# Performance work log

Measured on AMD Instinct MI355X. Metric: run time of the kernel, lower is better.

Reference implementation:

```python
import jax, jax.numpy as jnp
import numpy as np

T = 4096      # sentence length
V = 50257     # vocab size
E = 1024      # embedding dim
H = 512       # hidden per direction (hidden_dim // 2)
NT = 32       # tagset size


def setup_inputs() -> dict:
    key = jax.random.key(0)
    ks = jax.random.split(key, 12)
    s = 0.02
    return {
        "sentence": jax.random.randint(ks[0], (T,), 0, V, dtype=jnp.int32),
        "emb": jax.random.normal(ks[1], (V, E), jnp.float32) * s,
        "W_ih_f": jax.random.normal(ks[2], (3 * H, E), jnp.float32) * s,
        "W_hh_f": jax.random.normal(ks[3], (3 * H, H), jnp.float32) * s,
        "b_ih_f": jax.random.normal(ks[4], (3 * H,), jnp.float32) * s,
        "b_hh_f": jax.random.normal(ks[5], (3 * H,), jnp.float32) * s,
        "W_ih_b": jax.random.normal(ks[6], (3 * H, E), jnp.float32) * s,
        "W_hh_b": jax.random.normal(ks[7], (3 * H, H), jnp.float32) * s,
        "b_ih_b": jax.random.normal(ks[8], (3 * H,), jnp.float32) * s,
        "b_hh_b": jax.random.normal(ks[9], (3 * H,), jnp.float32) * s,
        "W_out": jax.random.normal(ks[10], (NT, E), jnp.float32) * s,
    }


def _gru_dir(x, W_ih, W_hh, b_ih, b_hh):
    """Run a single-direction GRU over x [T, E] -> hidden states [T, H].
    PyTorch GRU gate math: r,z,n order; h' = (1-z)*n + z*h; h0 = 0."""
    gi = x @ W_ih.T + b_ih  # [T, 3H] input projections, one big GEMM

    def step(h, gi_t):
        gh = h @ W_hh.T + b_hh            # [3H]
        ir, iz, inn = jnp.split(gi_t, 3)
        hr, hz, hn = jnp.split(gh, 3)
        r = jax.nn.sigmoid(ir + hr)
        z = jax.nn.sigmoid(iz + hz)
        n = jnp.tanh(inn + r * hn)
        h_new = (1.0 - z) * n + z * h
        return h_new, h_new

    h0 = jnp.zeros((W_hh.shape[1],), x.dtype)
    _, hs = jax.lax.scan(step, h0, gi)
    return hs  # [T, H]


def reference(sentence, emb, W_ih_f, W_hh_f, b_ih_f, b_hh_f,
              W_ih_b, W_hh_b, b_ih_b, b_hh_b, W_out):
    x = emb[sentence]  # [T, E] embedding lookup
    h_fwd = _gru_dir(x, W_ih_f, W_hh_f, b_ih_f, b_hh_f)            # [T, H]
    h_bwd = _gru_dir(x[::-1], W_ih_b, W_hh_b, b_ih_b, b_hh_b)[::-1]  # [T, H]
    h = jnp.concatenate([h_fwd, h_bwd], axis=-1)  # [T, 2H]
    return h @ W_out.T  # [T, NT] tag scores (no bias)
```

## Files before the change

kernel.cpp:

```cpp
#include <hip/hip_runtime.h>

#define T_LEN 4096
#define E_DIM 1024
#define H_DIM 512
#define NT_DIM 32
#define NG 3072
#define G_DIR 64
#define OPW 8

typedef __attribute__((ext_vector_type(8))) short bf16x8;
typedef __attribute__((ext_vector_type(4))) float f32x4;
typedef unsigned long long ull;

__device__ inline unsigned short f2bf(float f) {
    unsigned int u = __float_as_uint(f);
    unsigned int r = (u + 0x7fffu + ((u >> 16) & 1u)) >> 16;
    return (unsigned short)r;
}
__device__ inline float bf2f(unsigned short u) {
    return __uint_as_float(((unsigned int)u) << 16);
}
__device__ inline ull packhs(float v, unsigned tag) {
    return (ull)__float_as_uint(v) | ((ull)tag << 32);
}

__global__ void embed_cast(const int* __restrict__ sent, const float* __restrict__ emb,
                           unsigned short* __restrict__ xb) {
    int t = blockIdx.x;
    int row = sent[t];
    const float4* src = (const float4*)(emb + (size_t)row * E_DIM);
    ushort4* dst = (ushort4*)(xb + (size_t)t * E_DIM);
    float4 v = src[threadIdx.x];
    ushort4 o;
    o.x = f2bf(v.x); o.y = f2bf(v.y); o.z = f2bf(v.z); o.w = f2bf(v.w);
    dst[threadIdx.x] = o;
}

__global__ void wcast(const float* __restrict__ wf, const float* __restrict__ wb_,
                      unsigned short* __restrict__ w) {
    int r = blockIdx.x;
    const float* src = (r < 1536) ? (wf + (size_t)r * E_DIM) : (wb_ + (size_t)(r - 1536) * E_DIM);
    const float4* s4 = (const float4*)src;
    ushort4* dst = (ushort4*)(w + (size_t)r * E_DIM);
    float4 v = s4[threadIdx.x];
    ushort4 o;
    o.x = f2bf(v.x); o.y = f2bf(v.y); o.z = f2bf(v.z); o.w = f2bf(v.w);
    dst[threadIdx.x] = o;
}

#define LDST 40
__global__ __launch_bounds__(256) void gi_gemm(const unsigned short* __restrict__ xb,
                                               const unsigned short* __restrict__ wb,
                                               const float* __restrict__ bihf,
                                               const float* __restrict__ bihb,
                                               unsigned short* __restrict__ gi) {
    __shared__ __align__(16) unsigned short As[64 * LDST];
    __shared__ __align__(16) unsigned short Bs[64 * LDST];
    int tile_m = (blockIdx.x % 64) * 64;
    int tile_n = (blockIdx.x / 64) * 64;
    int tid = threadIdx.x;
    int lane = tid & 63, wv = tid >> 6;
    int quad = lane >> 4, r15 = lane & 15;
    int srow = tid >> 2, sseg = tid & 3;

    f32x4 acc[4] = {};
    for (int kb = 0; kb < E_DIM; kb += 32) {
        uint4 a = *(const uint4*)(xb + (size_t)(tile_m + srow) * E_DIM + kb + sseg * 8);
        uint4 b = *(const uint4*)(wb + (size_t)(tile_n + srow) * E_DIM + kb + sseg * 8);
        *(uint4*)&As[srow * LDST + sseg * 8] = a;
        *(uint4*)&Bs[srow * LDST + sseg * 8] = b;
        __syncthreads();
        bf16x8 af = *(bf16x8*)&As[(wv * 16 + r15) * LDST + quad * 8];
#pragma unroll
        for (int nt = 0; nt < 4; nt++) {
            bf16x8 bf = *(bf16x8*)&Bs[(nt * 16 + r15) * LDST + quad * 8];
            acc[nt] = __builtin_amdgcn_mfma_f32_16x16x32_bf16(af, bf, acc[nt], 0, 0, 0);
        }
        __syncthreads();
    }
#pragma unroll
    for (int nt = 0; nt < 4; nt++) {
        int gn = tile_n + nt * 16 + r15;
        float bias = (gn < 1536) ? bihf[gn] : bihb[gn - 1536];
#pragma unroll
        for (int rg = 0; rg < 4; rg++) {
            int gm = tile_m + wv * 16 + quad * 4 + rg;
            gi[(size_t)gm * NG + gn] = f2bf(acc[nt][rg] + bias);
        }
    }
}

__global__ __launch_bounds__(512) void gru_rec(
    const float* __restrict__ whhf, const float* __restrict__ bhhf,
    const float* __restrict__ whhb, const float* __restrict__ bhhb,
    const unsigned short* __restrict__ gi, ull* __restrict__ hxf, ull* __restrict__ hxb) {
    int wgid = blockIdx.x;
    int dir = wgid >> 6;
    int g = wgid & 63;
    const float* whh = dir ? whhb : whhf;
    const float* bhh = dir ? bhhb : bhhf;
    ull* hx = dir ? hxb : hxf;

    int tid = threadIdx.x;
    int kp = tid & 7;
    int q = tid >> 3;
    int kg = g * OPW + kp;
    int wave = tid >> 6;
    int lane = tid & 63;

    float4 wr[2], wz[2], wn[2];
    {
        const float4* pr_ = (const float4*)(whh + (size_t)kg * H_DIM + q * 8);
        const float4* pz_ = (const float4*)(whh + (size_t)(kg + 512) * H_DIM + q * 8);
        const float4* pn_ = (const float4*)(whh + (size_t)(kg + 1024) * H_DIM + q * 8);
        wr[0] = pr_[0]; wr[1] = pr_[1];
        wz[0] = pz_[0]; wz[1] = pz_[1];
        wn[0] = pn_[0]; wn[1] = pn_[1];
    }
    float bias_r = 0.f, bias_z = 0.f, bias_n = 0.f, h_own = 0.f;
    int kg0 = g * OPW + lane;
    if (wave == 0 && lane < OPW) {
        bias_r = bhh[kg0]; bias_z = bhh[kg0 + 512]; bias_n = bhh[kg0 + 1024];
    }

    __shared__ float hsh[512];
    __shared__ float part[3][8][OPW];
    hsh[tid] = 0.f;
    __syncthreads();

    float gir = 0.f, giz = 0.f, gin = 0.f;

    for (int s = 0; s < T_LEN; s++) {
        int row = dir ? (T_LEN - 1 - s) : s;
        if (wave == 0) {
            if (lane < OPW) {
                const unsigned short* gp = gi + (size_t)row * NG + dir * 1536 + kg0;
                gir = bf2f(gp[0]); giz = bf2f(gp[512]); gin = bf2f(gp[1024]);
            }
            if (s > 0) {
                int prow = dir ? (T_LEN - s) : (s - 1);
                const ull* rowp = hx + (size_t)prow * H_DIM;
                ull v[8];
                bool ok;
                do {
#pragma unroll
                    for (int i = 0; i < 8; i++)
                        v[i] = __hip_atomic_load(rowp + lane + 64 * i,
                                                 __ATOMIC_RELAXED, __HIP_MEMORY_SCOPE_AGENT);
                    ok = true;
#pragma unroll
                    for (int i = 0; i < 8; i++)
                        ok = ok && ((unsigned)(v[i] >> 32) == (unsigned)s);
                } while (!ok);
#pragma unroll
                for (int i = 0; i < 8; i++)
                    hsh[lane + 64 * i] = __uint_as_float((unsigned)v[i]);
            }
        }
        __syncthreads();

        float4 h0 = *(const float4*)&hsh[q * 8];
        float4 h1 = *(const float4*)&hsh[q * 8 + 4];
        float pr, pz, pn;
        pr  = wr[0].x * h0.x + wr[0].y * h0.y + wr[0].z * h0.z + wr[0].w * h0.w
            + wr[1].x * h1.x + wr[1].y * h1.y + wr[1].z * h1.z + wr[1].w * h1.w;
        pz  = wz[0].x * h0.x + wz[0].y * h0.y + wz[0].z * h0.z + wz[0].w * h0.w
            + wz[1].x * h1.x + wz[1].y * h1.y + wz[1].z * h1.z + wz[1].w * h1.w;
        pn  = wn[0].x * h0.x + wn[0].y * h0.y + wn[0].z * h0.z + wn[0].w * h0.w
            + wn[1].x * h1.x + wn[1].y * h1.y + wn[1].z * h1.z + wn[1].w * h1.w;
        pr += __shfl_xor(pr, 8);  pz += __shfl_xor(pz, 8);  pn += __shfl_xor(pn, 8);
        pr += __shfl_xor(pr, 16); pz += __shfl_xor(pz, 16); pn += __shfl_xor(pn, 16);
        pr += __shfl_xor(pr, 32); pz += __shfl_xor(pz, 32); pn += __shfl_xor(pn, 32);
        if (lane < OPW) {
            part[0][wave][lane] = pr; part[1][wave][lane] = pz; part[2][wave][lane] = pn;
        }
        __syncthreads();

        if (wave == 0 && lane < OPW) {
            float sr = bias_r, sz = bias_z, sn = bias_n;
#pragma unroll
            for (int w = 0; w < 8; w++) {
                sr += part[0][w][lane]; sz += part[1][w][lane]; sn += part[2][w][lane];
            }
            float rr = 1.f / (1.f + __expf(-(gir + sr)));
            float zz = 1.f / (1.f + __expf(-(giz + sz)));
            float a = gin + rr * sn;
            a = fminf(20.f, fmaxf(-20.f, a));
            float e = __expf(-2.f * a);
            float nn = (1.f - e) / (1.f + e);
            float hnew = (1.f - zz) * nn + zz * h_own;
            h_own = hnew;
            __hip_atomic_store(hx + (size_t)row * H_DIM + kg0, packhs(hnew, (unsigned)(s + 1)),
                               __ATOMIC_RELAXED, __HIP_MEMORY_SCOPE_AGENT);
        }
    }
}

__global__ __launch_bounds__(256) void out_gemm(const ull* __restrict__ hxf,
                                                const ull* __restrict__ hxb,
                                                const float* __restrict__ wout,
                                                float* __restrict__ out) {
    __shared__ __align__(16) float ls[8][1028];
    int t0 = blockIdx.x * 8;
    int tid = threadIdx.x;
#pragma unroll
    for (int i = 0; i < 8; i++) {
        int col = tid * 4;
        const ull* src = (col < 512) ? (hxf + (size_t)(t0 + i) * H_DIM + col)
                                     : (hxb + (size_t)(t0 + i) * H_DIM + (col - 512));
        ull s0 = src[0], s1 = src[1], s2 = src[2], s3 = src[3];
        ls[i][col + 0] = __uint_as_float((unsigned)s0);
        ls[i][col + 1] = __uint_as_float((unsigned)s1);
        ls[i][col + 2] = __uint_as_float((unsigned)s2);
        ls[i][col + 3] = __uint_as_float((unsigned)s3);
    }
    __syncthreads();
    int r8 = tid >> 5, gg = tid & 31;
    const float4* wp = (const float4*)(wout + (size_t)gg * 1024);
    float sum = 0.f;
#pragma unroll 8
    for (int j = 0; j < 256; j++) {
        float4 w = wp[j];
        float4 h = *(const float4*)&ls[r8][j * 4];
        sum += w.x * h.x + w.y * h.y + w.z * h.z + w.w * h.w;
    }
    out[(size_t)(t0 + r8) * NT_DIM + gg] = sum;
}

extern "C" void kernel_launch(void* const* d_in, const int* in_sizes, int n_in,
                              void* d_out, int out_size, void* d_ws, size_t ws_size,
                              hipStream_t stream) {
    const int*   sent = (const int*)d_in[0];
    const float* emb  = (const float*)d_in[1];
    const float* wihf = (const float*)d_in[2];
    const float* whhf = (const float*)d_in[3];
    const float* bihf = (const float*)d_in[4];
    const float* bhhf = (const float*)d_in[5];
    const float* wihb = (const float*)d_in[6];
    const float* whhb = (const float*)d_in[7];
    const float* bihb = (const float*)d_in[8];
    const float* bhhb = (const float*)d_in[9];
    const float* wout = (const float*)d_in[10];

    char* ws = (char*)d_ws;
    unsigned short* gi  = (unsigned short*)(ws);
    unsigned short* xb  = (unsigned short*)(ws + 25165824);
    unsigned short* wb  = (unsigned short*)(ws + 33554432);
    ull*            hxf = (ull*)(ws + 39845888);
    ull*            hxb = (ull*)(ws + 56623104);
    float*          out = (float*)d_out;

    embed_cast<<<T_LEN, 256, 0, stream>>>(sent, emb, xb);
    wcast<<<NG, 256, 0, stream>>>(wihf, wihb, wb);
    gi_gemm<<<64 * 48, 256, 0, stream>>>(xb, wb, bihf, bihb, gi);
    gru_rec<<<2 * G_DIR, 512, 0, stream>>>(whhf, bhhf, whhb, bhhb, gi, hxf, hxb);
    out_gemm<<<T_LEN / 8, 256, 0, stream>>>(hxf, hxb, wout, out);
}
```

Baseline: 6.238 ms.

## Run each GRU recurrence block as a single wavefront holding its weights in registers

Changes the recurrent kernel from 512-thread blocks to one 64-lane wave per block. Each lane keeps 192 weight floats in registers and covers a 64-wide slice of the hidden vector. The cross-wave partial-sum reduction through shared memory, and its extra barrier, is replaced by a three-step intra-wave shuffle. All lanes now poll the flag-tagged hidden state directly. This shortens the per-timestep critical path, but the very high register count per lane risks spills, and the loaded weights are less coalesced.

```diff
diff --git a/kernel.cpp b/kernel.cpp
--- a/kernel.cpp
+++ b/kernel.cpp
@@ -6,7 +6,6 @@
 #define NT_DIM 32
 #define NG 3072
 #define G_DIR 64
-#define OPW 8
 
 typedef __attribute__((ext_vector_type(8))) short bf16x8;
 typedef __attribute__((ext_vector_type(4))) float f32x4;
@@ -90,7 +89,7 @@
     }
 }
 
-__global__ __launch_bounds__(512) void gru_rec(
+__global__ __launch_bounds__(64, 1) void gru_rec(
     const float* __restrict__ whhf, const float* __restrict__ bhhf,
     const float* __restrict__ whhb, const float* __restrict__ bhhb,
     const unsigned short* __restrict__ gi, ull* __restrict__ hxf, ull* __restrict__ hxb) {
@@ -101,96 +100,80 @@
     const float* bhh = dir ? bhhb : bhhf;
     ull* hx = dir ? hxb : hxf;
 
-    int tid = threadIdx.x;
-    int kp = tid & 7;
-    int q = tid >> 3;
-    int kg = g * OPW + kp;
-    int wave = tid >> 6;
-    int lane = tid & 63;
-
-    float4 wr[2], wz[2], wn[2];
+    int l = threadIdx.x;
+    int p = l & 7;
+    int o = l >> 3;
+    int c = g * 8 + o;
+
+    float4 wr[16], wz[16], wn[16];
     {
-        const float4* pr_ = (const float4*)(whh + (size_t)kg * H_DIM + q * 8);
-        const float4* pz_ = (const float4*)(whh + (size_t)(kg + 512) * H_DIM + q * 8);
-        const float4* pn_ = (const float4*)(whh + (size_t)(kg + 1024) * H_DIM + q * 8);
-        wr[0] = pr_[0]; wr[1] = pr_[1];
-        wz[0] = pz_[0]; wz[1] = pz_[1];
-        wn[0] = pn_[0]; wn[1] = pn_[1];
+        const float4* r0 = (const float4*)(whh + (size_t)c * H_DIM + p * 64);
+        const float4* z0 = (const float4*)(whh + (size_t)(c + 512) * H_DIM + p * 64);
+        const float4* n0 = (const float4*)(whh + (size_t)(c + 1024) * H_DIM + p * 64);
+#pragma unroll
+        for (int j = 0; j < 16; j++) { wr[j] = r0[j]; wz[j] = z0[j]; wn[j] = n0[j]; }
     }
     float bias_r = 0.f, bias_z = 0.f, bias_n = 0.f, h_own = 0.f;
-    int kg0 = g * OPW + lane;
-    if (wave == 0 && lane < OPW) {
-        bias_r = bhh[kg0]; bias_z = bhh[kg0 + 512]; bias_n = bhh[kg0 + 1024];
-    }
-
-    __shared__ float hsh[512];
-    __shared__ float part[3][8][OPW];
-    hsh[tid] = 0.f;
+    if (p == 0) { bias_r = bhh[c]; bias_z = bhh[c + 512]; bias_n = bhh[c + 1024]; }
+
+    __shared__ float hsh[8 * 68];
+#pragma unroll
+    for (int i = 0; i < 8; i++) hsh[i * 68 + l] = 0.f;
     __syncthreads();
 
     float gir = 0.f, giz = 0.f, gin = 0.f;
 
     for (int s = 0; s < T_LEN; s++) {
         int row = dir ? (T_LEN - 1 - s) : s;
-        if (wave == 0) {
-            if (lane < OPW) {
-                const unsigned short* gp = gi + (size_t)row * NG + dir * 1536 + kg0;
-                gir = bf2f(gp[0]); giz = bf2f(gp[512]); gin = bf2f(gp[1024]);
-            }
-            if (s > 0) {
-                int prow = dir ? (T_LEN - s) : (s - 1);
-                const ull* rowp = hx + (size_t)prow * H_DIM;
-                ull v[8];
-                bool ok;
-                do {
-#pragma unroll
-                    for (int i = 0; i < 8; i++)
-                        v[i] = __hip_atomic_load(rowp + lane + 64 * i,
-                                                 __ATOMIC_RELAXED, __HIP_MEMORY_SCOPE_AGENT);
-                    ok = true;
-#pragma unroll
-                    for (int i = 0; i < 8; i++)
-                        ok = ok && ((unsigned)(v[i] >> 32) == (unsigned)s);
-                } while (!ok);
+        if (p == 0) {
+            const unsigned short* gp = gi + (size_t)row * NG + dir * 1536 + c;
+            gir = bf2f(gp[0]); giz = bf2f(gp[512]); gin = bf2f(gp[1024]);
+        }
+        if (s > 0) {
+            int prow = dir ? (T_LEN - s) : (s - 1);
+            const ull* rowp = hx + (size_t)prow * H_DIM;
+            ull v[8];
+            bool ok;
+            do {
 #pragma unroll
                 for (int i = 0; i < 8; i++)
-                    hsh[lane + 64 * i] = __uint_as_float((unsigned)v[i]);
-            }
+                    v[i] = __hip_atomic_load(rowp + l + 64 * i,
+                                             __ATOMIC_RELAXED, __HIP_MEMORY_SCOPE_AGENT);
+                ok = true;
+#pragma unroll
+                for (int i = 0; i < 8; i++)
+                    ok = ok && ((unsigned)(v[i] >> 32) == (unsigned)s);
+            } while (!ok);
+            __syncthreads();
+#pragma unroll
+            for (int i = 0; i < 8; i++)
+                hsh[i * 68 + l] = __uint_as_float((unsigned)v[i]);
         }
         __syncthreads();
 
-        float4 h0 = *(const float4*)&hsh[q * 8];
-        float4 h1 = *(const float4*)&hsh[q * 8 + 4];
-        float pr, pz, pn;
-        pr  = wr[0].x * h0.x + wr[0].y * h0.y + wr[0].z * h0.z + wr[0].w * h0.w
-            + wr[1].x * h1.x + wr[1].y * h1.y + wr[1].z * h1.z + wr[1].w * h1.w;
-        pz  = wz[0].x * h0.x + wz[0].y * h0.y + wz[0].z * h0.z + wz[0].w * h0.w
-            + wz[1].x * h1.x + wz[1].y * h1.y + wz[1].z * h1.z + wz[1].w * h1.w;
-        pn  = wn[0].x * h0.x + wn[0].y * h0.y + wn[0].z * h0.z + wn[0].w * h0.w
-            + wn[1].x * h1.x + wn[1].y * h1.y + wn[1].z * h1.z + wn[1].w * h1.w;
-        pr += __shfl_xor(pr, 8);  pz += __shfl_xor(pz, 8);  pn += __shfl_xor(pn, 8);
-        pr += __shfl_xor(pr, 16); pz += __shfl_xor(pz, 16); pn += __shfl_xor(pn, 16);
-        pr += __shfl_xor(pr, 32); pz += __shfl_xor(pz, 32); pn += __shfl_xor(pn, 32);
-        if (lane < OPW) {
-            part[0][wave][lane] = pr; part[1][wave][lane] = pz; part[2][wave][lane] = pn;
-        }
-        __syncthreads();
-
-        if (wave == 0 && lane < OPW) {
-            float sr = bias_r, sz = bias_z, sn = bias_n;
-#pragma unroll
-            for (int w = 0; w < 8; w++) {
-                sr += part[0][w][lane]; sz += part[1][w][lane]; sn += part[2][w][lane];
-            }
-            float rr = 1.f / (1.f + __expf(-(gir + sr)));
-            float zz = 1.f / (1.f + __expf(-(giz + sz)));
-            float a = gin + rr * sn;
+        float pr = 0.f, pz = 0.f, pn = 0.f;
+        const float* hb = &hsh[p * 68];
+#pragma unroll
+        for (int j = 0; j < 16; j++) {
+            float4 h4 = *(const float4*)(hb + j * 4);
+            pr += wr[j].x * h4.x + wr[j].y * h4.y + wr[j].z * h4.z + wr[j].w * h4.w;
+            pz += wz[j].x * h4.x + wz[j].y * h4.y + wz[j].z * h4.z + wz[j].w * h4.w;
+            pn += wn[j].x * h4.x + wn[j].y * h4.y + wn[j].z * h4.z + wn[j].w * h4.w;
+        }
+        pr += __shfl_xor(pr, 1);  pz += __shfl_xor(pz, 1);  pn += __shfl_xor(pn, 1);
+        pr += __shfl_xor(pr, 2);  pz += __shfl_xor(pz, 2);  pn += __shfl_xor(pn, 2);
+        pr += __shfl_xor(pr, 4);  pz += __shfl_xor(pz, 4);  pn += __shfl_xor(pn, 4);
+
+        if (p == 0) {
+            float rr = 1.f / (1.f + __expf(-(gir + pr + bias_r)));
+            float zz = 1.f / (1.f + __expf(-(giz + pz + bias_z)));
+            float a = gin + rr * (pn + bias_n);
             a = fminf(20.f, fmaxf(-20.f, a));
             float e = __expf(-2.f * a);
             float nn = (1.f - e) / (1.f + e);
             float hnew = (1.f - zz) * nn + zz * h_own;
             h_own = hnew;
-            __hip_atomic_store(hx + (size_t)row * H_DIM + kg0, packhs(hnew, (unsigned)(s + 1)),
+            __hip_atomic_store(hx + (size_t)row * H_DIM + c, packhs(hnew, (unsigned)(s + 1)),
                                __ATOMIC_RELAXED, __HIP_MEMORY_SCOPE_AGENT);
         }
     }
@@ -253,6 +236,6 @@
     embed_cast<<<T_LEN, 256, 0, stream>>>(sent, emb, xb);
     wcast<<<NG, 256, 0, stream>>>(wihf, wihb, wb);
     gi_gemm<<<64 * 48, 256, 0, stream>>>(xb, wb, bihf, bihb, gi);
-    gru_rec<<<2 * G_DIR, 512, 0, stream>>>(whhf, bhhf, whhb, bhhb, gi, hxf, hxb);
+    gru_rec<<<2 * G_DIR, 64, 0, stream>>>(whhf, bhhf, whhb, bhhb, gi, hxf, hxb);
     out_gemm<<<T_LEN / 8, 256, 0, stream>>>(hxf, hxb, wout, out);
 }
```

New measurement: 6.759 ms. 8.4% more time.
